# Optimization experiments

Measured on AMD Instinct MI355X. Metric: run time of the kernel, lower is better.

The kernel has to match this reference:

```python
import jax, jax.numpy as jnp
import numpy as np

B, SI, ST, C, H, D = 1, 1024, 256, 3072, 24, 128
MLP = 4 * C
EPS = 1e-6
SCALE = 1.0 / float(np.sqrt(D))


def _ln(x):
    m = jnp.mean(x, -1, keepdims=True)
    v = jnp.var(x, -1, keepdims=True)
    return (x - m) / jnp.sqrt(v + EPS)


def _rms(x, w):
    return x * jax.lax.rsqrt(jnp.mean(x * x, -1, keepdims=True) + EPS) * w


def _mod(x, shift, scale):
    # AdaLN modulation: x * (1 + scale) + shift, scale/shift are [B, C]
    return x * (1.0 + scale[:, None, :]) + shift[:, None, :]


def _rot_half(x):
    xr, xi = x[..., 0::2], x[..., 1::2]
    return jnp.stack([-xi, xr], -1).reshape(x.shape)


def _rope(x, cos, sin):
    # x: [B, S, H, D]; cos/sin: [S, D]
    return x * cos[None, :, None, :] + _rot_half(x) * sin[None, :, None, :]


def _forward(img, txt, vec, fc, fs,
             i_mod_w, i_mod_b, i_qkv_w, i_qkv_b, i_qn, i_kn, i_pw, i_pb, i_f1w, i_f1b, i_f2w, i_f2b,
             t_mod_w, t_mod_b, t_qkv_w, t_qkv_b, t_qn, t_kn, t_pw, t_pb, t_f1w, t_f1b, t_f2w, t_f2b):
    sv = jax.nn.silu(vec)
    i_s1, i_c1, i_g1, i_s2, i_c2, i_g2 = jnp.split(sv @ i_mod_w + i_mod_b, 6, -1)
    t_s1, t_c1, t_g1, t_s2, t_c2, t_g2 = jnp.split(sv @ t_mod_w + t_mod_b, 6, -1)

    # img stream: LN -> modulate -> QKV -> qk RMSNorm -> RoPE
    iqkv = (_mod(_ln(img), i_s1, i_c1) @ i_qkv_w + i_qkv_b).reshape(B, SI, 3, H, D)
    iq = _rope(_rms(iqkv[:, :, 0], i_qn), fc, fs)
    ik = _rope(_rms(iqkv[:, :, 1], i_kn), fc, fs)
    iv = iqkv[:, :, 2]

    # txt stream: no RoPE
    tqkv = (_mod(_ln(txt), t_s1, t_c1) @ t_qkv_w + t_qkv_b).reshape(B, ST, 3, H, D)
    tq = _rms(tqkv[:, :, 0], t_qn)
    tk = _rms(tqkv[:, :, 1], t_kn)
    tv = tqkv[:, :, 2]

    q = jnp.concatenate([iq, tq], 1)
    k = jnp.concatenate([ik, tk], 1)
    v = jnp.concatenate([iv, tv], 1)

    logits = jnp.einsum('bqhd,bkhd->bhqk', q, k) * SCALE
    o = jnp.einsum('bhqk,bkhd->bqhd', jax.nn.softmax(logits, -1), v).reshape(B, SI + ST, C)
    ia, ta = o[:, :SI], o[:, SI:]

    img = img + (ia @ i_pw + i_pb) * i_g1[:, None, :]
    h = jax.nn.gelu(_mod(_ln(img), i_s2, i_c2) @ i_f1w + i_f1b, approximate=True)
    img = img + (h @ i_f2w + i_f2b) * i_g2[:, None, :]

    txt = txt + (ta @ t_pw + t_pb) * t_g1[:, None, :]
    h = jax.nn.gelu(_mod(_ln(txt), t_s2, t_c2) @ t_f1w + t_f1b, approximate=True)
    txt = txt + (h @ t_f2w + t_f2b) * t_g2[:, None, :]
    return img, txt


def setup_inputs() -> dict:
    key = jax.random.key(0)
    ki = iter(jax.random.split(key, 32))

    def w(shape, s=0.02):
        return jax.random.normal(next(ki), shape, jnp.float32) * s

    # RoPE tables shaped (img_seq_len, head_dim), interleaved pair layout
    pos = jnp.arange(SI, dtype=jnp.float32)
    inv = 1.0 / (10000.0 ** (jnp.arange(0, D, 2, dtype=jnp.float32) / D))
    ang = pos[:, None] * inv[None, :]
    inp = dict(
        img=jax.random.normal(next(ki), (B, SI, C), jnp.float32),
        txt=jax.random.normal(next(ki), (B, ST, C), jnp.float32),
        vec=jax.random.normal(next(ki), (B, C), jnp.float32),
        freqs_cos=jnp.repeat(jnp.cos(ang), 2, -1),
        freqs_sin=jnp.repeat(jnp.sin(ang), 2, -1),
    )
    for p in ('i', 't'):
        inp[p + '_mod_w'] = w((C, 6 * C)); inp[p + '_mod_b'] = jnp.zeros((6 * C,), jnp.float32)
        inp[p + '_qkv_w'] = w((C, 3 * C)); inp[p + '_qkv_b'] = jnp.zeros((3 * C,), jnp.float32)
        inp[p + '_qn'] = jnp.ones((D,), jnp.float32); inp[p + '_kn'] = jnp.ones((D,), jnp.float32)
        inp[p + '_pw'] = w((C, C)); inp[p + '_pb'] = jnp.zeros((C,), jnp.float32)
        inp[p + '_f1w'] = w((C, MLP)); inp[p + '_f1b'] = jnp.zeros((MLP,), jnp.float32)
        inp[p + '_f2w'] = w((MLP, C)); inp[p + '_f2b'] = jnp.zeros((C,), jnp.float32)
    return inp


def reference(img, txt, vec, freqs_cos, freqs_sin,
              i_mod_w, i_mod_b, i_qkv_w, i_qkv_b, i_qn, i_kn, i_pw, i_pb, i_f1w, i_f1b, i_f2w, i_f2b,
              t_mod_w, t_mod_b, t_qkv_w, t_qkv_b, t_qn, t_kn, t_pw, t_pb, t_f1w, t_f1b, t_f2w, t_f2b):
    return _forward(img, txt, vec, freqs_cos, freqs_sin,
                    i_mod_w, i_mod_b, i_qkv_w, i_qkv_b, i_qn, i_kn, i_pw, i_pb, i_f1w, i_f1b, i_f2w, i_f2b,
                    t_mod_w, t_mod_b, t_qkv_w, t_qkv_b, t_qn, t_kn, t_pw, t_pb, t_f1w, t_f1b, t_f2w, t_f2b)
```

## Files before the change

kernel.cpp:

```cpp
#include <hip/hip_runtime.h>


#define SI 1024
#define ST 256
#define SS 1280
#define CC 3072
#define NH 24
#define DH 128
#define MLPD 12288
#define EPSF 1e-6f
#define SCALEF 0.08838834764831845f

typedef __attribute__((ext_vector_type(4))) float f32x4;
typedef __attribute__((ext_vector_type(8))) __bf16 bf16x8;
typedef unsigned short u16;
typedef unsigned int u32;

__device__ __forceinline__ u16 f2bf(float x) {
    union { float f; u32 u; } v; v.f = x;
    u32 r = v.u + 0x7FFFu + ((v.u >> 16) & 1u);
    return (u16)(r >> 16);
}

__device__ __forceinline__ int gsw(int r) {
    return ((r >> 2) & 7) ^ ((r & 3) << 1);
}

__global__ __launch_bounds__(256) void k_modvec(
    const float* __restrict__ vec,
    const float* __restrict__ wi, const float* __restrict__ bi,
    const float* __restrict__ wt, const float* __restrict__ bt,
    float* __restrict__ mi, float* __restrict__ mt)
{
    __shared__ float sv[CC];
    __shared__ float part[7][128];
    int t = threadIdx.x;
    for (int i = t; i < CC; i += 256) {
        float x = vec[i];
        sv[i] = x / (1.f + __expf(-x));
    }
    __syncthreads();
    int gc = blockIdx.x;
    int strm = gc >= 144;
    const float* W  = strm ? wt : wi;
    const float* Bv = strm ? bt : bi;
    float* out      = strm ? mt : mi;
    int c0 = (gc % 144) * 128 + 4 * (t & 31);
    int g  = t >> 5;
    const float* wp  = W + (size_t)(g * 384) * (6 * CC) + c0;
    const float* svp = sv + g * 384;
    f32x4 acc = {0.f, 0.f, 0.f, 0.f};
    for (int r = 0; r < 384; ++r) {
        f32x4 wr = *(const f32x4*)(wp + (size_t)r * (6 * CC));
        float s = svp[r];
        acc.x += wr.x * s; acc.y += wr.y * s; acc.z += wr.z * s; acc.w += wr.w * s;
    }
    int li = t & 31;
    if (g > 0) *(f32x4*)&part[g - 1][li * 4] = acc;
    __syncthreads();
    if (g == 0) {
#pragma unroll
        for (int i = 0; i < 7; ++i) {
            f32x4 p = *(const f32x4*)&part[i][li * 4];
            acc.x += p.x; acc.y += p.y; acc.z += p.z; acc.w += p.w;
        }
        f32x4 bb = *(const f32x4*)(Bv + c0);
        acc.x += bb.x; acc.y += bb.y; acc.z += bb.z; acc.w += bb.w;
        *(f32x4*)(out + c0) = acc;
    }
}

__global__ __launch_bounds__(256) void k_lnmod(
    const float* __restrict__ x,
    const float* __restrict__ shift, const float* __restrict__ scale,
    u16* __restrict__ out)
{
    int r = blockIdx.x;
    const float* xp = x + (size_t)r * CC;
    u16* op = out + (size_t)r * CC;
    int t = threadIdx.x;
    float4 v[3];
    float s = 0.f, q = 0.f;
#pragma unroll
    for (int j = 0; j < 3; ++j) {
        v[j] = *(const float4*)(xp + j * 1024 + t * 4);
        s += v[j].x + v[j].y + v[j].z + v[j].w;
        q += v[j].x * v[j].x + v[j].y * v[j].y + v[j].z * v[j].z + v[j].w * v[j].w;
    }
#pragma unroll
    for (int m = 32; m; m >>= 1) { s += __shfl_xor(s, m); q += __shfl_xor(q, m); }
    __shared__ float red[8];
    int w = t >> 6;
    if ((t & 63) == 0) { red[w] = s; red[4 + w] = q; }
    __syncthreads();
    s = red[0] + red[1] + red[2] + red[3];
    q = red[4] + red[5] + red[6] + red[7];
    float mean = s * (1.f / CC);
    float var  = q * (1.f / CC) - mean * mean;
    float inv  = rsqrtf(var + EPSF);
#pragma unroll
    for (int j = 0; j < 3; ++j) {
        int c0 = j * 1024 + t * 4;
        float4 sh = *(const float4*)(shift + c0);
        float4 sc = *(const float4*)(scale + c0);
        ushort4 o;
        o.x = f2bf((v[j].x - mean) * inv * (1.f + sc.x) + sh.x);
        o.y = f2bf((v[j].y - mean) * inv * (1.f + sc.y) + sh.y);
        o.z = f2bf((v[j].z - mean) * inv * (1.f + sc.z) + sh.z);
        o.w = f2bf((v[j].w - mean) * inv * (1.f + sc.w) + sh.w);
        *(ushort4*)(op + c0) = o;
    }
}

template <int V, int BN>
__global__ __launch_bounds__(512, 2) void k_gemm(
    const u16* __restrict__ A,
    const float* __restrict__ Wi, const float* __restrict__ Wt,
    const float* __restrict__ bi, const float* __restrict__ bt,
    void* __restrict__ outv, int MBI, int N, int K, int lda)
{
    constexpr int BM  = 256;
    constexpr int NWN = (BN == 256) ? 4 : 2;
    constexpr int WM  = (BN == 256) ? 128 : 64;
    constexpr int MI  = WM / 16;
    constexpr int NFB = (BN == 256) ? 8 : 4;

    __shared__ u16 lA[2][BM * 64];
    __shared__ u16 lB[2][BN * 64];
    int t = threadIdx.x;
    int m0 = blockIdx.y * BM;
    int n0 = blockIdx.x * BN;
    bool txts = (blockIdx.y >= (unsigned)MBI);
    const float* W = txts ? Wt : Wi;
    const size_t koff = (size_t)blockIdx.z * K;

    int w = t >> 6, lane = t & 63;
    int wm = (w / NWN) * WM, wn = (w % NWN) * 64;
    int lr = lane & 15, lg = lane >> 4;

    f32x4 acc[MI][4];
#pragma unroll
    for (int i = 0; i < MI; ++i)
#pragma unroll
        for (int j = 0; j < 4; ++j) acc[i][j] = (f32x4){0.f, 0.f, 0.f, 0.f};

    const int bn4 = (BN == 256) ? 4 * (t & 63) : 4 * (t & 31);
    const int bk  = (BN == 256) ? 8 * (t >> 6) : 4 * (t >> 5);
    f32x4 fb[NFB];
    const int NT = K >> 6;

    auto LOADB = [&](int kt) {
        size_t kb = koff + (size_t)kt * 64 + bk;
#pragma unroll
        for (int i = 0; i < NFB; ++i)
            fb[i] = *(const f32x4*)(W + (kb + i) * (size_t)N + n0 + bn4);
    };
    auto GLDSA = [&](int kt, int buf) {
        size_t kb = koff + (size_t)kt * 64;
#pragma unroll
        for (int i = 0; i < 4; ++i) {
            int D = i * 512 + t; int row = D >> 3;
            int c = (D & 7) ^ gsw(row);
            const u16* gp = A + (size_t)(m0 + row) * lda + kb + c * 8;
            u16* lp = &lA[buf][D * 8];
            __builtin_amdgcn_global_load_lds(
                (const __attribute__((address_space(1))) void*)gp,
                (__attribute__((address_space(3))) void*)lp, 16, 0, 0);
        }
    };
    auto CVTWR = [&](int buf) {
        if constexpr (BN == 256) {
#pragma unroll
            for (int j = 0; j < 4; ++j) {
                int n = bn4 + j;
                union { uint4 q; __bf16 h[8]; } u;
#pragma unroll
                for (int i = 0; i < 8; ++i) u.h[i] = (__bf16)fb[i][j];
                int cp = (bk >> 3) ^ gsw(n);
                *(uint4*)&lB[buf][n * 64 + cp * 8] = u.q;
            }
        } else {
#pragma unroll
            for (int j = 0; j < 4; ++j) {
                int n = bn4 + j;
                union { uint2 q; __bf16 h[4]; } u;
#pragma unroll
                for (int i = 0; i < 4; ++i) u.h[i] = (__bf16)fb[i][j];
                int cp = (bk >> 3) ^ gsw(n);
                *(uint2*)&lB[buf][n * 64 + cp * 8 + (bk & 4)] = u.q;
            }
        }
    };
    auto MFMAP = [&](int buf) {
#pragma unroll
        for (int ks = 0; ks < 2; ++ks) {
            bf16x8 bv[4];
#pragma unroll
            for (int j = 0; j < 4; ++j) {
                int n = wn + j * 16 + lr;
                bv[j] = *(const bf16x8*)&lB[buf][n * 64 + (((ks * 4 + lg) ^ gsw(n)) * 8)];
            }
#pragma unroll
            for (int mh = 0; mh < MI / 4; ++mh) {
                bf16x8 af[4];
#pragma unroll
                for (int i2 = 0; i2 < 4; ++i2) {
                    int m = wm + (mh * 4 + i2) * 16 + lr;
                    af[i2] = *(const bf16x8*)&lA[buf][m * 64 + (((ks * 4 + lg) ^ gsw(m)) * 8)];
                }
                __builtin_amdgcn_s_setprio(1);
#pragma unroll
                for (int i2 = 0; i2 < 4; ++i2)
#pragma unroll
                    for (int j = 0; j < 4; ++j)
                        acc[mh * 4 + i2][j] = __builtin_amdgcn_mfma_f32_16x16x32_bf16(
                            af[i2], bv[j], acc[mh * 4 + i2][j], 0, 0, 0);
                __builtin_amdgcn_s_setprio(0);
            }
        }
    };
    auto VMWN = [&]() {
        if constexpr (BN == 256)
            asm volatile("s_waitcnt vmcnt(8) lgkmcnt(0)" ::: "memory");
        else
            asm volatile("s_waitcnt vmcnt(4) lgkmcnt(0)" ::: "memory");
    };

    LOADB(0);
    GLDSA(0, 0);
    CVTWR(0);
    if (NT > 1) LOADB(1);
    VMWN();
    __builtin_amdgcn_s_barrier();
    __builtin_amdgcn_sched_barrier(0);

    int cur = 0;
    for (int kt = 0; kt < NT; ++kt) {
        bool s1 = kt + 1 < NT;
        bool s2 = kt + 2 < NT;
        if (s1) {
            GLDSA(kt + 1, cur ^ 1);
            CVTWR(cur ^ 1);
        }
        if (s2) LOADB(kt + 2);
        MFMAP(cur);
        if (s1) {
            if (s2) { VMWN(); }
            else    { asm volatile("s_waitcnt vmcnt(0) lgkmcnt(0)" ::: "memory"); }
            __builtin_amdgcn_s_barrier();
            __builtin_amdgcn_sched_barrier(0);
        }
        cur ^= 1;
    }

    const float* Bb = txts ? bt : bi;
    int MT = gridDim.y * BM;
#pragma unroll
    for (int i = 0; i < MI; ++i) {
#pragma unroll
        for (int j = 0; j < 4; ++j) {
            int col = n0 + wn + j * 16 + lr;
            float bvv = (V == 3) ? 0.f : Bb[col];
#pragma unroll
            for (int e = 0; e < 4; ++e) {
                int row = m0 + wm + i * 16 + lg * 4 + e;
                float val = acc[i][j][e] + bvv;
                if (V == 0) {
                    ((float*)outv)[(size_t)row * N + col] = val;
                } else if (V == 1) {
                    float g = 0.5f * val * (1.f + tanhf(0.7978845608028654f * (val + 0.044715f * val * val * val)));
                    ((u16*)outv)[(size_t)row * N + col] = f2bf(g);
                } else {
                    ((float*)outv)[((size_t)blockIdx.z * MT + row) * N + col] = val;
                }
            }
        }
    }
}

__global__ __launch_bounds__(256) void k_red(
    const float* __restrict__ p,
    const float* __restrict__ bi, const float* __restrict__ bt,
    const float* __restrict__ gi, const float* __restrict__ gt,
    const float* __restrict__ basei, const float* __restrict__ baset,
    float* __restrict__ out)
{
    int idx4 = blockIdx.x * 256 + threadIdx.x;
    size_t idx = (size_t)idx4 * 4;
    const size_t MN = (size_t)SS * CC;
    int r = idx4 / 768;
    int c = (idx4 - r * 768) * 4;
    bool ts = r >= SI;
    float4 v0 = *(const float4*)(p + idx);
    float4 v1 = *(const float4*)(p + MN + idx);
    float4 bb = *(const float4*)((ts ? bt : bi) + c);
    float4 gg = *(const float4*)((ts ? gt : gi) + c);
    const float* bp = ts ? (baset + (size_t)(r - SI) * CC + c) : (basei + (size_t)r * CC + c);
    float4 ba = *(const float4*)bp;
    float4 o;
    o.x = ba.x + (v0.x + v1.x + bb.x) * gg.x;
    o.y = ba.y + (v0.y + v1.y + bb.y) * gg.y;
    o.z = ba.z + (v0.z + v1.z + bb.z) * gg.z;
    o.w = ba.w + (v0.w + v1.w + bb.w) * gg.w;
    *(float4*)(out + idx) = o;
}

__global__ __launch_bounds__(256) void k_pack(
    const float* __restrict__ qkv,
    const float* __restrict__ iqn, const float* __restrict__ ikn,
    const float* __restrict__ tqn, const float* __restrict__ tkn,
    const float* __restrict__ fc, const float* __restrict__ fs,
    u16* __restrict__ qpk, u16* __restrict__ kpk, u16* __restrict__ vpk)
{
    int wid = blockIdx.x * 4 + (threadIdx.x >> 6);
    int lane = threadIdx.x & 63;
    int s = wid / 72;
    int wh = wid % 72;
    int which = wh / 24;
    int h = wh % 24;
    int d = lane * 2;
    const float* src = qkv + (size_t)s * 9216 + which * 3072 + h * 128 + d;
    float x0 = src[0], x1 = src[1];
    float y0 = x0, y1 = x1;
    if (which < 2) {
        float ssq = x0 * x0 + x1 * x1;
#pragma unroll
        for (int m = 32; m; m >>= 1) ssq += __shfl_xor(ssq, m);
        float inv = rsqrtf(ssq * (1.f / 128.f) + EPSF);
        bool isimg = (s < SI);
        const float* wv = (which == 0) ? (isimg ? iqn : tqn) : (isimg ? ikn : tkn);
        y0 = x0 * inv * wv[d];
        y1 = x1 * inv * wv[d + 1];
        if (isimg) {
            float c0 = fc[s * 128 + d], c1 = fc[s * 128 + d + 1];
            float s0 = fs[s * 128 + d], s1 = fs[s * 128 + d + 1];
            float r0 = y0 * c0 - y1 * s0;
            float r1 = y1 * c1 + y0 * s1;
            y0 = r0; y1 = r1;
        }
        if (which == 0) { y0 *= SCALEF; y1 *= SCALEF; }
    }
    u16* dst = (which == 0) ? qpk : (which == 1) ? kpk : vpk;
    ushort2 o; o.x = f2bf(y0); o.y = f2bf(y1);
    *(ushort2*)(dst + ((size_t)h * SS + s) * 128 + d) = o;
}

__global__ __launch_bounds__(512, 1) void k_attn(
    const u16* __restrict__ qpk, const u16* __restrict__ kpk,
    const u16* __restrict__ vpk, u16* __restrict__ o)
{
    __shared__ u16 lK[128 * 136];
    __shared__ u16 lV[128 * 136];
    __shared__ u16 lP[128 * 136];
    int h = blockIdx.y;
    int q0 = blockIdx.x * 128;
    int t = threadIdx.x, w = t >> 6, lane = t & 63;
    int lr = lane & 15, lg = lane >> 4;
    const u16* qh = qpk + (size_t)h * SS * 128;
    const u16* kh = kpk + (size_t)h * SS * 128;
    const u16* vh = vpk + (size_t)h * SS * 128;

    bf16x8 aq[4];
#pragma unroll
    for (int kk = 0; kk < 4; ++kk)
        aq[kk] = *(const bf16x8*)(qh + (size_t)(q0 + w * 16 + lr) * 128 + kk * 32 + lg * 8);

    const f32x4 fz = {0.f, 0.f, 0.f, 0.f};
    f32x4 oa[8];
#pragma unroll
    for (int j = 0; j < 8; ++j) oa[j] = fz;
    float mrow[4], lrow[4];
#pragma unroll
    for (int e = 0; e < 4; ++e) { mrow[e] = -1e30f; lrow[e] = 0.f; }

    for (int kt = 0; kt < 10; ++kt) {
        int t0 = kt * 128;
        __syncthreads();
#pragma unroll
        for (int it = 0; it < 4; ++it) {
            int c = it * 512 + t;
            int row = c >> 4, part = c & 15;
            uint4 d4 = *(const uint4*)(kh + (size_t)(t0 + row) * 128 + part * 8);
            *(uint4*)(&lK[row * 136 + part * 8]) = d4;
        }
#pragma unroll
        for (int it = 0; it < 2; ++it) {
            int c = it * 512 + t;
            int pr = c >> 4;
            int tt = pr * 2;
            int k = c & 15;
            int d0 = k * 8;
            uint4 a = *(const uint4*)(vh + (size_t)(t0 + tt) * 128 + d0);
            uint4 b = *(const uint4*)(vh + (size_t)(t0 + tt + 1) * 128 + d0);
            const u16* a16 = (const u16*)&a;
            const u16* b16 = (const u16*)&b;
            int ts = tt ^ ((k & 7) << 3);
#pragma unroll
            for (int j = 0; j < 8; ++j) {
                ushort2 pv; pv.x = a16[j]; pv.y = b16[j];
                *(ushort2*)(&lV[(d0 + j) * 136 + ts]) = pv;
            }
        }
        __syncthreads();
        f32x4 sa[8];
#pragma unroll
        for (int j = 0; j < 8; ++j) sa[j] = fz;
#pragma unroll
        for (int kk = 0; kk < 4; ++kk) {
            bf16x8 bk[8];
#pragma unroll
            for (int ni = 0; ni < 8; ++ni)
                bk[ni] = *(const bf16x8*)(&lK[(ni * 16 + lr) * 136 + kk * 32 + lg * 8]);
#pragma unroll
            for (int ni = 0; ni < 8; ++ni)
                sa[ni] = __builtin_amdgcn_mfma_f32_16x16x32_bf16(aq[kk], bk[ni], sa[ni], 0, 0, 0);
        }
#pragma unroll
        for (int e = 0; e < 4; ++e) {
            float mx = sa[0][e];
#pragma unroll
            for (int ni = 1; ni < 8; ++ni) mx = fmaxf(mx, sa[ni][e]);
#pragma unroll
            for (int msk = 1; msk < 16; msk <<= 1) mx = fmaxf(mx, __shfl_xor(mx, msk));
            float mnew = fmaxf(mrow[e], mx);
            float esc = __expf(mrow[e] - mnew);
            mrow[e] = mnew;
            float rsum = 0.f;
#pragma unroll
            for (int ni = 0; ni < 8; ++ni) {
                float p = __expf(sa[ni][e] - mnew);
                sa[ni][e] = p;
                rsum += p;
            }
#pragma unroll
            for (int msk = 1; msk < 16; msk <<= 1) rsum += __shfl_xor(rsum, msk);
            lrow[e] = lrow[e] * esc + rsum;
#pragma unroll
            for (int nd = 0; nd < 8; ++nd) oa[nd][e] *= esc;
        }
#pragma unroll
        for (int ni = 0; ni < 8; ++ni)
#pragma unroll
            for (int e = 0; e < 4; ++e)
                lP[(w * 16 + lg * 4 + e) * 136 + ni * 16 + lr] = f2bf(sa[ni][e]);
#pragma unroll
        for (int kk = 0; kk < 4; ++kk) {
            bf16x8 pa, vb[8];
            pa = *(const bf16x8*)(&lP[(w * 16 + lr) * 136 + kk * 32 + lg * 8]);
#pragma unroll
            for (int nd = 0; nd < 8; ++nd) {
                int d = nd * 16 + lr;
                int ch = (kk * 4 + lg) ^ ((d >> 3) & 7);
                vb[nd] = *(const bf16x8*)(&lV[d * 136 + ch * 8]);
            }
#pragma unroll
            for (int nd = 0; nd < 8; ++nd)
                oa[nd] = __builtin_amdgcn_mfma_f32_16x16x32_bf16(pa, vb[nd], oa[nd], 0, 0, 0);
        }
    }
#pragma unroll
    for (int nd = 0; nd < 8; ++nd) {
#pragma unroll
        for (int e = 0; e < 4; ++e) {
            int row = q0 + w * 16 + lg * 4 + e;
            int col = h * 128 + nd * 16 + lr;
            o[(size_t)row * CC + col] = f2bf(oa[nd][e] / lrow[e]);
        }
    }
}

extern "C" void kernel_launch(void* const* d_in, const int* in_sizes, int n_in,
                              void* d_out, int out_size, void* d_ws, size_t ws_size,
                              hipStream_t stream)
{
    const float* img  = (const float*)d_in[0];
    const float* txt  = (const float*)d_in[1];
    const float* vec  = (const float*)d_in[2];
    const float* fc   = (const float*)d_in[3];
    const float* fs   = (const float*)d_in[4];
    const float* i_mod_w = (const float*)d_in[5];
    const float* i_mod_b = (const float*)d_in[6];
    const float* i_qkv_w = (const float*)d_in[7];
    const float* i_qkv_b = (const float*)d_in[8];
    const float* i_qn  = (const float*)d_in[9];
    const float* i_kn  = (const float*)d_in[10];
    const float* i_pw  = (const float*)d_in[11];
    const float* i_pb  = (const float*)d_in[12];
    const float* i_f1w = (const float*)d_in[13];
    const float* i_f1b = (const float*)d_in[14];
    const float* i_f2w = (const float*)d_in[15];
    const float* i_f2b = (const float*)d_in[16];
    const float* t_mod_w = (const float*)d_in[17];
    const float* t_mod_b = (const float*)d_in[18];
    const float* t_qkv_w = (const float*)d_in[19];
    const float* t_qkv_b = (const float*)d_in[20];
    const float* t_qn  = (const float*)d_in[21];
    const float* t_kn  = (const float*)d_in[22];
    const float* t_pw  = (const float*)d_in[23];
    const float* t_pb  = (const float*)d_in[24];
    const float* t_f1w = (const float*)d_in[25];
    const float* t_f1b = (const float*)d_in[26];
    const float* t_f2w = (const float*)d_in[27];
    const float* t_f2b = (const float*)d_in[28];

    char* ws = (char*)d_ws;
    float* mod_i = (float*)(ws + 0);
    float* mod_t = (float*)(ws + 73728);
    u16*   xmod  = (u16*)(ws + 147456);
    float* qkv   = (float*)(ws + 8011776);
    u16*   qpk   = (u16*)(ws + 55197696);
    u16*   kpk   = (u16*)(ws + 63062016);
    u16*   vpk   = (u16*)(ws + 70926336);
    u16*   obuf  = (u16*)(ws + 78790656);
    u16*   hbuf  = (u16*)(ws + 8011776);
    float* pbufP = (float*)(ws + 8011776);
    float* pbufF = (float*)(ws + 39469056);

    float* out_img = (float*)d_out;
    float* out_txt = out_img + (size_t)SI * CC;

    k_modvec<<<288, 256, 0, stream>>>(vec, i_mod_w, i_mod_b, t_mod_w, t_mod_b, mod_i, mod_t);

    k_lnmod<<<SI, 256, 0, stream>>>(img, mod_i + 0, mod_i + 3072, xmod);
    k_lnmod<<<ST, 256, 0, stream>>>(txt, mod_t + 0, mod_t + 3072, xmod + (size_t)SI * CC);

    k_gemm<0, 256><<<dim3(36, 5, 1), 512, 0, stream>>>(xmod, i_qkv_w, t_qkv_w, i_qkv_b, t_qkv_b,
                                                       qkv, 4, 9216, CC, CC);

    k_pack<<<23040, 256, 0, stream>>>(qkv, i_qn, i_kn, t_qn, t_kn, fc, fs, qpk, kpk, vpk);

    k_attn<<<dim3(10, 24), 512, 0, stream>>>(qpk, kpk, vpk, obuf);

    k_gemm<3, 128><<<dim3(24, 5, 2), 512, 0, stream>>>(obuf, i_pw, t_pw, nullptr, nullptr,
                                                       pbufP, 4, CC, CC / 2, CC);
    k_red<<<3840, 256, 0, stream>>>(pbufP, i_pb, t_pb, mod_i + 6144, mod_t + 6144,
                                    img, txt, out_img);

    k_lnmod<<<SI, 256, 0, stream>>>(out_img, mod_i + 9216, mod_i + 12288, xmod);
    k_lnmod<<<ST, 256, 0, stream>>>(out_txt, mod_t + 9216, mod_t + 12288, xmod + (size_t)SI * CC);

    k_gemm<1, 256><<<dim3(48, 5, 1), 512, 0, stream>>>(xmod, i_f1w, t_f1w, i_f1b, t_f1b,
                                                       hbuf, 4, MLPD, CC, CC);

    k_gemm<3, 128><<<dim3(24, 5, 2), 512, 0, stream>>>(hbuf, i_f2w, t_f2w, nullptr, nullptr,
                                                       pbufF, 4, CC, MLPD / 2, MLPD);
    k_red<<<3840, 256, 0, stream>>>(pbufF, i_f2b, t_f2b, mod_i + 15360, mod_t + 15360,
                                    out_img, out_txt, out_img);
}
```

Measured before the change: 667.0 us.

## Add 8-wave ping-pong GEMM with interleaved loads and MFMA phases for BN=256

Adds a separate k_gemm8 kernel for the QKV and FC1 GEMMs. It splits each k-tile into four phases and spreads the weight fp32 loads, A global-to-LDS loads and bf16 conversion writes across those phases, with barriers between the LDS reads and MFMA bursts. The goal is to hide global-load and conversion latency behind matrix math instead of issuing all loads at the start of each tile. The original GEMM is specialised to the BN=128 split-K path only. The extra barriers add synchronisation overhead and may lower throughput if the waves do not overlap well.

Result: slower. 882.7 us (+32.3%).

```diff
diff --git a/kernel.cpp b/kernel.cpp
--- a/kernel.cpp
+++ b/kernel.cpp
@@ -112,19 +112,177 @@
     }
 }
 
-template <int V, int BN>
+template <int V>
+__global__ __launch_bounds__(512, 2) void k_gemm8(
+    const u16* __restrict__ A,
+    const float* __restrict__ Wi, const float* __restrict__ Wt,
+    const float* __restrict__ bi, const float* __restrict__ bt,
+    void* __restrict__ outv, int MBI, int N, int K, int lda)
+{
+    __shared__ u16 lA[2][256 * 64];
+    __shared__ u16 lB[2][256 * 64];
+    int t = threadIdx.x;
+    int m0 = blockIdx.y * 256;
+    int n0 = blockIdx.x * 256;
+    bool txts = (blockIdx.y >= (unsigned)MBI);
+    const float* W = txts ? Wt : Wi;
+
+    int w = t >> 6, lane = t & 63;
+    int wm = (w >> 2) * 128, wn = (w & 3) * 64;
+    int lr = lane & 15, lg = lane >> 4;
+
+    f32x4 acc[8][4];
+#pragma unroll
+    for (int i = 0; i < 8; ++i)
+#pragma unroll
+        for (int j = 0; j < 4; ++j) acc[i][j] = (f32x4){0.f, 0.f, 0.f, 0.f};
+
+    const int bn4 = 4 * (t & 63);
+    const int bk  = 8 * (t >> 6);
+    f32x4 fb[8];
+    const int NT = K >> 6;
+
+    auto LOADB_H = [&](int kt, int h) {
+        size_t kb = (size_t)kt * 64 + bk;
+#pragma unroll
+        for (int i = 0; i < 4; ++i)
+            fb[h * 4 + i] = *(const f32x4*)(W + (kb + h * 4 + i) * (size_t)N + n0 + bn4);
+    };
+    auto GLDSA_H = [&](int kt, int buf, int h) {
+        size_t kb = (size_t)kt * 64;
+#pragma unroll
+        for (int i = 0; i < 2; ++i) {
+            int D = (h * 2 + i) * 512 + t; int row = D >> 3;
+            int c = (D & 7) ^ gsw(row);
+            const u16* gp = A + (size_t)(m0 + row) * lda + kb + c * 8;
+            u16* lp = &lA[buf][D * 8];
+            __builtin_amdgcn_global_load_lds(
+                (const __attribute__((address_space(1))) void*)gp,
+                (__attribute__((address_space(3))) void*)lp, 16, 0, 0);
+        }
+    };
+    auto CVTWR = [&](int buf) {
+#pragma unroll
+        for (int j = 0; j < 4; ++j) {
+            int n = bn4 + j;
+            union { uint4 q; __bf16 h[8]; } u;
+#pragma unroll
+            for (int i = 0; i < 8; ++i) u.h[i] = (__bf16)fb[i][j];
+            int cp = (bk >> 3) ^ gsw(n);
+            *(uint4*)&lB[buf][n * 64 + cp * 8] = u.q;
+        }
+    };
+    auto RDQ = [&](int buf, int mh, int ks, bf16x8* bv, bf16x8* af) {
+#pragma unroll
+        for (int j = 0; j < 4; ++j) {
+            int n = wn + j * 16 + lr;
+            bv[j] = *(const bf16x8*)&lB[buf][n * 64 + (((ks * 4 + lg) ^ gsw(n)) * 8)];
+        }
+#pragma unroll
+        for (int i = 0; i < 4; ++i) {
+            int m = wm + (mh * 4 + i) * 16 + lr;
+            af[i] = *(const bf16x8*)&lA[buf][m * 64 + (((ks * 4 + lg) ^ gsw(m)) * 8)];
+        }
+    };
+    auto MM = [&](int mh, bf16x8* bv, bf16x8* af) {
+        __builtin_amdgcn_s_setprio(1);
+#pragma unroll
+        for (int i = 0; i < 4; ++i)
+#pragma unroll
+            for (int j = 0; j < 4; ++j)
+                acc[mh * 4 + i][j] = __builtin_amdgcn_mfma_f32_16x16x32_bf16(
+                    af[i], bv[j], acc[mh * 4 + i][j], 0, 0, 0);
+        __builtin_amdgcn_s_setprio(0);
+    };
+
+#define BARRIER __builtin_amdgcn_s_barrier()
+#define LGKM0 asm volatile("s_waitcnt lgkmcnt(0)" ::: "memory")
+#define SB0 __builtin_amdgcn_sched_barrier(0)
+
+    LOADB_H(0, 0); LOADB_H(0, 1);
+    GLDSA_H(0, 0, 0); GLDSA_H(0, 0, 1);
+    CVTWR(0);
+    LOADB_H(1, 0); LOADB_H(1, 1);
+    asm volatile("s_waitcnt vmcnt(8) lgkmcnt(0)" ::: "memory");
+    BARRIER; SB0;
+
+    int cur = 0;
+    for (int kt = 0; kt < NT; ++kt) {
+        bool s1 = kt + 1 < NT;
+        bool s2 = kt + 2 < NT;
+        {
+            bf16x8 bv[4], af[4];
+            RDQ(cur, 0, 0, bv, af);
+            if (s1) CVTWR(cur ^ 1);
+            BARRIER; LGKM0; SB0;
+            MM(0, bv, af);
+            BARRIER;
+        }
+        {
+            bf16x8 bv[4], af[4];
+            RDQ(cur, 0, 1, bv, af);
+            if (s1) GLDSA_H(kt + 1, cur ^ 1, 0);
+            if (s2) LOADB_H(kt + 2, 0);
+            BARRIER; LGKM0; SB0;
+            MM(0, bv, af);
+            BARRIER;
+        }
+        {
+            bf16x8 bv[4], af[4];
+            RDQ(cur, 1, 0, bv, af);
+            if (s1) GLDSA_H(kt + 1, cur ^ 1, 1);
+            if (s2) LOADB_H(kt + 2, 1);
+            BARRIER; LGKM0; SB0;
+            MM(1, bv, af);
+            BARRIER;
+        }
+        {
+            bf16x8 bv[4], af[4];
+            RDQ(cur, 1, 1, bv, af);
+            BARRIER; LGKM0; SB0;
+            MM(1, bv, af);
+            if (s1) {
+                if (s2) asm volatile("s_waitcnt vmcnt(4)" ::: "memory");
+                else    asm volatile("s_waitcnt vmcnt(0)" ::: "memory");
+                BARRIER; SB0;
+            }
+        }
+        cur ^= 1;
+    }
+#undef BARRIER
+#undef LGKM0
+#undef SB0
+
+    const float* Bb = txts ? bt : bi;
+#pragma unroll
+    for (int i = 0; i < 8; ++i) {
+#pragma unroll
+        for (int j = 0; j < 4; ++j) {
+            int col = n0 + wn + j * 16 + lr;
+            float bvv = Bb[col];
+#pragma unroll
+            for (int e = 0; e < 4; ++e) {
+                int row = m0 + wm + i * 16 + lg * 4 + e;
+                float val = acc[i][j][e] + bvv;
+                if (V == 0) {
+                    ((float*)outv)[(size_t)row * N + col] = val;
+                } else {
+                    float g = 0.5f * val * (1.f + tanhf(0.7978845608028654f * (val + 0.044715f * val * val * val)));
+                    ((u16*)outv)[(size_t)row * N + col] = f2bf(g);
+                }
+            }
+        }
+    }
+}
+
+template <int V>
 __global__ __launch_bounds__(512, 2) void k_gemm(
     const u16* __restrict__ A,
     const float* __restrict__ Wi, const float* __restrict__ Wt,
     const float* __restrict__ bi, const float* __restrict__ bt,
     void* __restrict__ outv, int MBI, int N, int K, int lda)
 {
-    constexpr int BM  = 256;
-    constexpr int NWN = (BN == 256) ? 4 : 2;
-    constexpr int WM  = (BN == 256) ? 128 : 64;
-    constexpr int MI  = WM / 16;
-    constexpr int NFB = (BN == 256) ? 8 : 4;
-
+    constexpr int BM = 256, BN = 128;
     __shared__ u16 lA[2][BM * 64];
     __shared__ u16 lB[2][BN * 64];
     int t = threadIdx.x;
@@ -135,24 +293,24 @@
     const size_t koff = (size_t)blockIdx.z * K;
 
     int w = t >> 6, lane = t & 63;
-    int wm = (w / NWN) * WM, wn = (w % NWN) * 64;
+    int wm = (w >> 1) * 64, wn = (w & 1) * 64;
     int lr = lane & 15, lg = lane >> 4;
 
-    f32x4 acc[MI][4];
-#pragma unroll
-    for (int i = 0; i < MI; ++i)
+    f32x4 acc[4][4];
+#pragma unroll
+    for (int i = 0; i < 4; ++i)
 #pragma unroll
         for (int j = 0; j < 4; ++j) acc[i][j] = (f32x4){0.f, 0.f, 0.f, 0.f};
 
-    const int bn4 = (BN == 256) ? 4 * (t & 63) : 4 * (t & 31);
-    const int bk  = (BN == 256) ? 8 * (t >> 6) : 4 * (t >> 5);
-    f32x4 fb[NFB];
+    const int bn4 = 4 * (t & 31);
+    const int bk  = 4 * (t >> 5);
+    f32x4 fb[4];
     const int NT = K >> 6;
 
     auto LOADB = [&](int kt) {
         size_t kb = koff + (size_t)kt * 64 + bk;
 #pragma unroll
-        for (int i = 0; i < NFB; ++i)
+        for (int i = 0; i < 4; ++i)
             fb[i] = *(const f32x4*)(W + (kb + i) * (size_t)N + n0 + bn4);
     };
     auto GLDSA = [&](int kt, int buf) {
@@ -169,26 +327,14 @@
         }
     };
     auto CVTWR = [&](int buf) {
-        if constexpr (BN == 256) {
-#pragma unroll
-            for (int j = 0; j < 4; ++j) {
-                int n = bn4 + j;
-                union { uint4 q; __bf16 h[8]; } u;
-#pragma unroll
-                for (int i = 0; i < 8; ++i) u.h[i] = (__bf16)fb[i][j];
-                int cp = (bk >> 3) ^ gsw(n);
-                *(uint4*)&lB[buf][n * 64 + cp * 8] = u.q;
-            }
-        } else {
-#pragma unroll
-            for (int j = 0; j < 4; ++j) {
-                int n = bn4 + j;
-                union { uint2 q; __bf16 h[4]; } u;
-#pragma unroll
-                for (int i = 0; i < 4; ++i) u.h[i] = (__bf16)fb[i][j];
-                int cp = (bk >> 3) ^ gsw(n);
-                *(uint2*)&lB[buf][n * 64 + cp * 8 + (bk & 4)] = u.q;
-            }
+#pragma unroll
+        for (int j = 0; j < 4; ++j) {
+            int n = bn4 + j;
+            union { uint2 q; __bf16 h[4]; } u;
+#pragma unroll
+            for (int i = 0; i < 4; ++i) u.h[i] = (__bf16)fb[i][j];
+            int cp = (bk >> 3) ^ gsw(n);
+            *(uint2*)&lB[buf][n * 64 + cp * 8 + (bk & 4)] = u.q;
         }
     };
     auto MFMAP = [&](int buf) {
@@ -200,37 +346,28 @@
                 int n = wn + j * 16 + lr;
                 bv[j] = *(const bf16x8*)&lB[buf][n * 64 + (((ks * 4 + lg) ^ gsw(n)) * 8)];
             }
-#pragma unroll
-            for (int mh = 0; mh < MI / 4; ++mh) {
-                bf16x8 af[4];
-#pragma unroll
-                for (int i2 = 0; i2 < 4; ++i2) {
-                    int m = wm + (mh * 4 + i2) * 16 + lr;
-                    af[i2] = *(const bf16x8*)&lA[buf][m * 64 + (((ks * 4 + lg) ^ gsw(m)) * 8)];
-                }
-                __builtin_amdgcn_s_setprio(1);
-#pragma unroll
-                for (int i2 = 0; i2 < 4; ++i2)
-#pragma unroll
-                    for (int j = 0; j < 4; ++j)
-                        acc[mh * 4 + i2][j] = __builtin_amdgcn_mfma_f32_16x16x32_bf16(
-                            af[i2], bv[j], acc[mh * 4 + i2][j], 0, 0, 0);
-                __builtin_amdgcn_s_setprio(0);
-            }
-        }
-    };
-    auto VMWN = [&]() {
-        if constexpr (BN == 256)
-            asm volatile("s_waitcnt vmcnt(8) lgkmcnt(0)" ::: "memory");
-        else
-            asm volatile("s_waitcnt vmcnt(4) lgkmcnt(0)" ::: "memory");
+            bf16x8 af[4];
+#pragma unroll
+            for (int i2 = 0; i2 < 4; ++i2) {
+                int m = wm + i2 * 16 + lr;
+                af[i2] = *(const bf16x8*)&lA[buf][m * 64 + (((ks * 4 + lg) ^ gsw(m)) * 8)];
+            }
+            __builtin_amdgcn_s_setprio(1);
+#pragma unroll
+            for (int i2 = 0; i2 < 4; ++i2)
+#pragma unroll
+                for (int j = 0; j < 4; ++j)
+                    acc[i2][j] = __builtin_amdgcn_mfma_f32_16x16x32_bf16(
+                        af[i2], bv[j], acc[i2][j], 0, 0, 0);
+            __builtin_amdgcn_s_setprio(0);
+        }
     };
 
     LOADB(0);
     GLDSA(0, 0);
     CVTWR(0);
     if (NT > 1) LOADB(1);
-    VMWN();
+    asm volatile("s_waitcnt vmcnt(4) lgkmcnt(0)" ::: "memory");
     __builtin_amdgcn_s_barrier();
     __builtin_amdgcn_sched_barrier(0);
 
@@ -245,34 +382,24 @@
         if (s2) LOADB(kt + 2);
         MFMAP(cur);
         if (s1) {
-            if (s2) { VMWN(); }
-            else    { asm volatile("s_waitcnt vmcnt(0) lgkmcnt(0)" ::: "memory"); }
+            if (s2) asm volatile("s_waitcnt vmcnt(4) lgkmcnt(0)" ::: "memory");
+            else    asm volatile("s_waitcnt vmcnt(0) lgkmcnt(0)" ::: "memory");
             __builtin_amdgcn_s_barrier();
             __builtin_amdgcn_sched_barrier(0);
         }
         cur ^= 1;
     }
 
-    const float* Bb = txts ? bt : bi;
     int MT = gridDim.y * BM;
 #pragma unroll
-    for (int i = 0; i < MI; ++i) {
+    for (int i = 0; i < 4; ++i) {
 #pragma unroll
         for (int j = 0; j < 4; ++j) {
             int col = n0 + wn + j * 16 + lr;
-            float bvv = (V == 3) ? 0.f : Bb[col];
 #pragma unroll
             for (int e = 0; e < 4; ++e) {
                 int row = m0 + wm + i * 16 + lg * 4 + e;
-                float val = acc[i][j][e] + bvv;
-                if (V == 0) {
-                    ((float*)outv)[(size_t)row * N + col] = val;
-                } else if (V == 1) {
-                    float g = 0.5f * val * (1.f + tanhf(0.7978845608028654f * (val + 0.044715f * val * val * val)));
-                    ((u16*)outv)[(size_t)row * N + col] = f2bf(g);
-                } else {
-                    ((float*)outv)[((size_t)blockIdx.z * MT + row) * N + col] = val;
-                }
+                ((float*)outv)[((size_t)blockIdx.z * MT + row) * N + col] = acc[i][j][e];
             }
         }
     }
@@ -524,26 +651,26 @@
     k_lnmod<<<SI, 256, 0, stream>>>(img, mod_i + 0, mod_i + 3072, xmod);
     k_lnmod<<<ST, 256, 0, stream>>>(txt, mod_t + 0, mod_t + 3072, xmod + (size_t)SI * CC);
 
-    k_gemm<0, 256><<<dim3(36, 5, 1), 512, 0, stream>>>(xmod, i_qkv_w, t_qkv_w, i_qkv_b, t_qkv_b,
-                                                       qkv, 4, 9216, CC, CC);
+    k_gemm8<0><<<dim3(36, 5, 1), 512, 0, stream>>>(xmod, i_qkv_w, t_qkv_w, i_qkv_b, t_qkv_b,
+                                                   qkv, 4, 9216, CC, CC);
 
     k_pack<<<23040, 256, 0, stream>>>(qkv, i_qn, i_kn, t_qn, t_kn, fc, fs, qpk, kpk, vpk);
 
     k_attn<<<dim3(10, 24), 512, 0, stream>>>(qpk, kpk, vpk, obuf);
 
-    k_gemm<3, 128><<<dim3(24, 5, 2), 512, 0, stream>>>(obuf, i_pw, t_pw, nullptr, nullptr,
-                                                       pbufP, 4, CC, CC / 2, CC);
+    k_gemm<3><<<dim3(24, 5, 2), 512, 0, stream>>>(obuf, i_pw, t_pw, nullptr, nullptr,
+                                                  pbufP, 4, CC, CC / 2, CC);
     k_red<<<3840, 256, 0, stream>>>(pbufP, i_pb, t_pb, mod_i + 6144, mod_t + 6144,
                                     img, txt, out_img);
 
     k_lnmod<<<SI, 256, 0, stream>>>(out_img, mod_i + 9216, mod_i + 12288, xmod);
     k_lnmod<<<ST, 256, 0, stream>>>(out_txt, mod_t + 9216, mod_t + 12288, xmod + (size_t)SI * CC);
 
-    k_gemm<1, 256><<<dim3(48, 5, 1), 512, 0, stream>>>(xmod, i_f1w, t_f1w, i_f1b, t_f1b,
-                                                       hbuf, 4, MLPD, CC, CC);
-
-    k_gemm<3, 128><<<dim3(24, 5, 2), 512, 0, stream>>>(hbuf, i_f2w, t_f2w, nullptr, nullptr,
-                                                       pbufF, 4, CC, MLPD / 2, MLPD);
+    k_gemm8<1><<<dim3(48, 5, 1), 512, 0, stream>>>(xmod, i_f1w, t_f1w, i_f1b, t_f1b,
+                                                   hbuf, 4, MLPD, CC, CC);
+
+    k_gemm<3><<<dim3(24, 5, 2), 512, 0, stream>>>(hbuf, i_f2w, t_f2w, nullptr, nullptr,
+                                                  pbufF, 4, CC, MLPD / 2, MLPD);
     k_red<<<3840, 256, 0, stream>>>(pbufF, i_f2b, t_f2b, mod_i + 15360, mod_t + 15360,
                                     out_img, out_txt, out_img);
 }
```
